# Optimization experiments

Measured on AMD Instinct MI355X. Metric: run time of the kernel, lower is better.

The kernel has to match this reference:

```python
import jax, jax.numpy as jnp
import numpy as np

D_MODEL = 2048
NUM_HEADS = 32
NUM_KV_HEADS = 8
D_K = D_MODEL // NUM_HEADS  # 64
GROUPS = NUM_HEADS // NUM_KV_HEADS  # 4
KV_DIM = NUM_KV_HEADS * D_K  # 512


def setup_inputs() -> dict:
    key = jax.random.key(0)
    ks = jax.random.split(key, 9)
    s = 0.02
    return {
        "x": jax.random.normal(ks[0], (2, 2048, D_MODEL), dtype=jnp.float32),
        "Wq": jax.random.normal(ks[1], (D_MODEL, D_MODEL), dtype=jnp.float32) * s,
        "bq": jnp.zeros((D_MODEL,), dtype=jnp.float32),
        "Wk": jax.random.normal(ks[2], (D_MODEL, KV_DIM), dtype=jnp.float32) * s,
        "bk": jnp.zeros((KV_DIM,), dtype=jnp.float32),
        "Wv": jax.random.normal(ks[3], (D_MODEL, KV_DIM), dtype=jnp.float32) * s,
        "bv": jnp.zeros((KV_DIM,), dtype=jnp.float32),
        "Wo": jax.random.normal(ks[4], (D_MODEL, D_MODEL), dtype=jnp.float32) * s,
        "bo": jnp.zeros((D_MODEL,), dtype=jnp.float32),
    }


def reference(x, Wq, bq, Wk, bk, Wv, bv, Wo, bo):
    B, S, _ = x.shape
    # projections
    Q = (x @ Wq + bq).reshape(B, S, NUM_HEADS, D_K).transpose(0, 2, 1, 3)      # [B,H,S,dk]
    K = (x @ Wk + bk).reshape(B, S, NUM_KV_HEADS, D_K).transpose(0, 2, 1, 3)   # [B,Hkv,S,dk]
    V = (x @ Wv + bv).reshape(B, S, NUM_KV_HEADS, D_K).transpose(0, 2, 1, 3)
    # repeat_interleave KV heads to match query heads
    K = jnp.repeat(K, GROUPS, axis=1)  # [B,H,S,dk]
    V = jnp.repeat(V, GROUPS, axis=1)
    scale = 1.0 / jnp.sqrt(jnp.asarray(D_K, dtype=x.dtype))
    scores = jnp.einsum("bhqd,bhkd->bhqk", Q, K) * scale  # [B,H,S,S]
    attn = jax.nn.softmax(scores, axis=-1)
    out = jnp.einsum("bhqk,bhkd->bhqd", attn, V)           # [B,H,S,dk]
    out = out.transpose(0, 2, 1, 3).reshape(B, S, D_MODEL)
    return out @ Wo + bo
```

## Files before the change

kernel.cpp:

```cpp
#include <hip/hip_runtime.h>
#include <hip/hip_bf16.h>
#include <stdint.h>

typedef __bf16 bf16;
typedef __bf16 bf16x8 __attribute__((ext_vector_type(8)));
typedef float  f32x2  __attribute__((ext_vector_type(2)));
typedef float  f32x4  __attribute__((ext_vector_type(4)));
typedef float  f32x16 __attribute__((ext_vector_type(16)));

#define D_MODEL 2048
#define KV_DIM  512
#define SEQ     2048
#define BATCH   2
#define MTOT    (BATCH*SEQ)
#define QKV_N   3072
#define QSCALE  (0.125f*1.44269504088896f)

#if __has_builtin(__builtin_amdgcn_exp2f)
#define EXP2(x) __builtin_amdgcn_exp2f(x)
#else
#define EXP2(x) exp2f(x)
#endif

__global__ __launch_bounds__(256) void cvt_f32_bf16(const float* __restrict__ in,
                                                    bf16* __restrict__ out, int n) {
  int i = (blockIdx.x * 256 + threadIdx.x) * 4;
  if (i < n) {
    float4 v = *reinterpret_cast<const float4*>(in + i);
    bf16 o[4] = {(bf16)v.x, (bf16)v.y, (bf16)v.z, (bf16)v.w};
    *reinterpret_cast<uint64_t*>(out + i) = *reinterpret_cast<const uint64_t*>(o);
  }
}

__global__ __launch_bounds__(256) void transpose_all(
    const float* __restrict__ Wq, const float* __restrict__ Wk,
    const float* __restrict__ Wv, const float* __restrict__ Wo,
    bf16* __restrict__ Wall, bf16* __restrict__ Wot) {
  const int z = blockIdx.z;
  const float* W; bf16* dst; int N;
  if (z == 0)      { W = Wq; dst = Wall;                          N = 2048; }
  else if (z == 1) { W = Wk; dst = Wall + (size_t)2048 * 2048;    N = 512;  }
  else if (z == 2) { W = Wv; dst = Wall + (size_t)2560 * 2048;    N = 512;  }
  else             { W = Wo; dst = Wot;                           N = 2048; }
  const int n0 = blockIdx.x * 64, k0 = blockIdx.y * 64;
  if (n0 >= N) return;
  __shared__ float tile[64][65];
  const int tx = threadIdx.x & 63;
  const int ty = threadIdx.x >> 6;
  #pragma unroll
  for (int i = ty; i < 64; i += 4)
    tile[i][tx] = W[(size_t)(k0 + i) * N + n0 + tx];
  __syncthreads();
  #pragma unroll
  for (int i = ty; i < 64; i += 4)
    dst[(size_t)(n0 + i) * 2048 + k0 + tx] = (bf16)tile[tx][i];
}

__global__ __launch_bounds__(256) void transpose_v(const bf16* __restrict__ QKV,
                                                   bf16* __restrict__ Vtg) {
  __shared__ bf16 t[64][72];
  const int st = blockIdx.x;
  const int bk = blockIdx.y;
  const int b = bk >> 3, kvh = bk & 7;
  const int tid = threadIdx.x;
  const int r = tid >> 2, c = (tid & 3) * 16;
  const bf16* src = QKV + (size_t)(b * SEQ + st * 64 + r) * QKV_N + 2560 + kvh * 64 + c;
  *(bf16x8*)&t[r][c]     = *(const bf16x8*)src;
  *(bf16x8*)&t[r][c + 8] = *(const bf16x8*)(src + 8);
  __syncthreads();
  bf16 tmp[16];
  #pragma unroll
  for (int j = 0; j < 16; ++j) tmp[j] = t[c + j][r];
  bf16* dst = Vtg + (size_t)(bk * 64 + r) * SEQ + st * 64 + c;
  *(bf16x8*)dst       = *(const bf16x8*)tmp;
  *(bf16x8*)(dst + 8) = *(const bf16x8*)(tmp + 8);
}

__device__ __forceinline__ void gload_lds16(const bf16* g, bf16* l) {
  __builtin_amdgcn_global_load_lds(
      (const __attribute__((address_space(1))) uint32_t*)g,
      (__attribute__((address_space(3))) uint32_t*)l, 16, 0, 0);
}

__device__ __forceinline__ uint32_t pk2(float a, float b) {
  union { bf16 h[2]; uint32_t u; } v;
  v.h[0] = (bf16)a; v.h[1] = (bf16)b;
  return v.u;
}

template<int OUT_BF16>
__global__ __launch_bounds__(256) void gemm_bt(
    const bf16* __restrict__ A, const bf16* __restrict__ Bt,
    const float* __restrict__ b0, const float* __restrict__ b1,
    const float* __restrict__ b2, int sp1, int sp2, int nscale, float scale,
    void* __restrict__ Cout, int M, int N, int K)
{
  __shared__ bf16 As[128 * 64];
  __shared__ bf16 Bs[128 * 64];
  const int tid  = threadIdx.x;
  const int lane = tid & 63;
  const int wid  = tid >> 6;
  const int wr = wid >> 1, wc = wid & 1;
  const int m0 = blockIdx.y * 128, n0 = blockIdx.x * 128;

  f32x4 acc[4][4] = {};

  const int srow = lane >> 3;
  const int scol = (lane & 7) * 8;

  for (int k0 = 0; k0 < K; k0 += 64) {
    #pragma unroll
    for (int i = 0; i < 4; ++i) {
      const int c = wid * 4 + i;
      gload_lds16(A  + (size_t)(m0 + c * 8 + srow) * K + k0 + scol, &As[c * 512]);
      gload_lds16(Bt + (size_t)(n0 + c * 8 + srow) * K + k0 + scol, &Bs[c * 512]);
    }
    __syncthreads();
    #pragma unroll
    for (int kk = 0; kk < 2; ++kk) {
      bf16x8 af[4], bfr[4];
      #pragma unroll
      for (int m = 0; m < 4; ++m)
        af[m] = *reinterpret_cast<const bf16x8*>(
            &As[(wr * 64 + m * 16 + (lane & 15)) * 64 + kk * 32 + (lane >> 4) * 8]);
      #pragma unroll
      for (int n = 0; n < 4; ++n)
        bfr[n] = *reinterpret_cast<const bf16x8*>(
            &Bs[(wc * 64 + n * 16 + (lane & 15)) * 64 + kk * 32 + (lane >> 4) * 8]);
      __builtin_amdgcn_s_setprio(1);
      #pragma unroll
      for (int m = 0; m < 4; ++m)
        #pragma unroll
        for (int n = 0; n < 4; ++n)
          acc[m][n] = __builtin_amdgcn_mfma_f32_16x16x32_bf16(af[m], bfr[n], acc[m][n], 0, 0, 0);
      __builtin_amdgcn_s_setprio(0);
    }
    __syncthreads();
  }

  const int rbase = m0 + wr * 64 + (lane >> 4) * 4;
  const int cbase = n0 + wc * 64 + (lane & 15);
  #pragma unroll
  for (int n = 0; n < 4; ++n) {
    const int col = cbase + n * 16;
    float bv;
    if (col < sp1)      bv = b0[col];
    else if (col < sp2) bv = b1[col - sp1];
    else                bv = b2[col - sp2];
    const float scl = (col < nscale) ? scale : 1.0f;
    #pragma unroll
    for (int m = 0; m < 4; ++m) {
      const int rb = rbase + m * 16;
      #pragma unroll
      for (int r = 0; r < 4; ++r) {
        const float v = (acc[m][n][r] + bv) * scl;
        if (OUT_BF16) ((bf16*)Cout)[(size_t)(rb + r) * N + col] = (bf16)v;
        else          ((float*)Cout)[(size_t)(rb + r) * N + col] = v;
      }
    }
  }
}

__global__ __launch_bounds__(256) void attn_kernel(
    const bf16* __restrict__ QKV, const bf16* __restrict__ Vtg, bf16* __restrict__ ctx)
{
  __shared__ bf16 smem[4][64 * 64];

  const int tid = threadIdx.x, lane = tid & 63, wid = tid >> 6;
  const int l31 = lane & 31, hi = lane >> 5;
  const int qt = blockIdx.x & 15;
  const int bh = blockIdx.x >> 4;
  const int h = bh & 31, b = bh >> 5, kvh = h >> 2;

  const bf16* gK = QKV + (size_t)b * SEQ * QKV_N + 2048 + kvh * 64;
  const bf16* gV = Vtg + (size_t)(b * 8 + kvh) * 64 * SEQ;

  const int sr  = lane >> 3;
  const int scn = (lane & 7) ^ sr;

  bf16x8 qf[4];
  {
    const bf16* qp = QKV + (size_t)(b * SEQ + qt * 128 + wid * 32 + l31) * QKV_N + h * 64 + hi * 8;
    #pragma unroll
    for (int kt = 0; kt < 4; ++kt) qf[kt] = *(const bf16x8*)(qp + kt * 16);
  }

  bf16x8 onesv;
  #pragma unroll
  for (int j = 0; j < 8; ++j) onesv[j] = (bf16)1.0f;

  f32x16 o0 = {}, o1 = {};
  f32x16 lacc = {};

  const int row0 = (wid * 2 + 0) * 8 + sr;
  const int row1 = (wid * 2 + 1) * 8 + sr;
  const bf16* pK0 = gK + (size_t)row0 * QKV_N + scn * 8;
  const bf16* pK1 = gK + (size_t)row1 * QKV_N + scn * 8;
  const bf16* pV0 = gV + (size_t)row0 * SEQ + scn * 8;
  const bf16* pV1 = gV + (size_t)row1 * SEQ + scn * 8;

  gload_lds16(pK0, &smem[0][(wid * 2 + 0) * 512]);
  gload_lds16(pK1, &smem[0][(wid * 2 + 1) * 512]);
  gload_lds16(pV0, &smem[2][(wid * 2 + 0) * 512]);
  gload_lds16(pV1, &smem[2][(wid * 2 + 1) * 512]);
  pK0 += (size_t)64 * QKV_N; pK1 += (size_t)64 * QKV_N; pV0 += 64; pV1 += 64;
  __syncthreads();

  const int rx = l31 & 7;

  for (int it = 0; it < 32; ++it) {
    const int cur = it & 1;
    if (it < 31) {
      gload_lds16(pK0, &smem[cur ^ 1][(wid * 2 + 0) * 512]);
      gload_lds16(pK1, &smem[cur ^ 1][(wid * 2 + 1) * 512]);
      gload_lds16(pV0, &smem[2 + (cur ^ 1)][(wid * 2 + 0) * 512]);
      gload_lds16(pV1, &smem[2 + (cur ^ 1)][(wid * 2 + 1) * 512]);
      pK0 += (size_t)64 * QKV_N; pK1 += (size_t)64 * QKV_N; pV0 += 64; pV1 += 64;
    }
    const bf16* Kb = smem[cur];
    const bf16* Vb = smem[2 + cur];

    bf16x8 kf[8];
    #pragma unroll
    for (int kt = 0; kt < 4; ++kt) {
      const int ck = hi + 2 * kt;
      kf[kt]     = *(const bf16x8*)(Kb + (size_t)l31 * 64        + ((ck ^ rx) * 8));
      kf[kt + 4] = *(const bf16x8*)(Kb + (size_t)(32 + l31) * 64 + ((ck ^ rx) * 8));
    }
    f32x16 s0v = {}, s1v = {};
    __builtin_amdgcn_s_setprio(1);
    #pragma unroll
    for (int kt = 0; kt < 4; ++kt) {
      s0v = __builtin_amdgcn_mfma_f32_32x32x16_bf16(kf[kt],     qf[kt], s0v, 0, 0, 0);
      s1v = __builtin_amdgcn_mfma_f32_32x32x16_bf16(kf[kt + 4], qf[kt], s1v, 0, 0, 0);
    }
    __builtin_amdgcn_s_setprio(0);

    bf16x8 vf[8];
    #pragma unroll
    for (int s = 0; s < 4; ++s) {
      const int ck = hi + 2 * s;
      vf[s]     = *(const bf16x8*)(Vb + (size_t)l31 * 64        + ((ck ^ rx) * 8));
      vf[s + 4] = *(const bf16x8*)(Vb + (size_t)(32 + l31) * 64 + ((ck ^ rx) * 8));
    }

    #pragma unroll
    for (int r = 0; r < 16; ++r) { s0v[r] = EXP2(s0v[r]); s1v[r] = EXP2(s1v[r]); }

    #pragma unroll
    for (int s = 0; s < 4; ++s) {
      const f32x16& sv = (s < 2) ? s0v : s1v;
      const int rb = (s & 1) * 8;
      uint32_t Aw = pk2(sv[rb + 0], sv[rb + 1]);
      uint32_t Bw = pk2(sv[rb + 2], sv[rb + 3]);
      uint32_t Cw = pk2(sv[rb + 4], sv[rb + 5]);
      uint32_t Dw = pk2(sv[rb + 6], sv[rb + 7]);
      union { uint32_t w[4]; bf16x8 v; } pf;
#if __has_builtin(__builtin_amdgcn_permlane32_swap)
      auto rA = __builtin_amdgcn_permlane32_swap(Aw, Cw, false, false);
      auto rB = __builtin_amdgcn_permlane32_swap(Bw, Dw, false, false);
      pf.w[0] = rA[0]; pf.w[1] = rB[0]; pf.w[2] = rA[1]; pf.w[3] = rB[1];
#else
      uint32_t U = hi ? Aw : Cw;
      uint32_t W = hi ? Bw : Dw;
      uint32_t pU = (uint32_t)__shfl_xor((int)U, 32);
      uint32_t pW = (uint32_t)__shfl_xor((int)W, 32);
      pf.w[0] = hi ? pU : Aw;
      pf.w[1] = hi ? pW : Bw;
      pf.w[2] = hi ? Cw : pU;
      pf.w[3] = hi ? Dw : pW;
#endif
      __builtin_amdgcn_s_setprio(1);
      o0 = __builtin_amdgcn_mfma_f32_32x32x16_bf16(vf[s],     pf.v, o0, 0, 0, 0);
      o1 = __builtin_amdgcn_mfma_f32_32x32x16_bf16(vf[s + 4], pf.v, o1, 0, 0, 0);
      lacc = __builtin_amdgcn_mfma_f32_32x32x16_bf16(onesv,   pf.v, lacc, 0, 0, 0);
      __builtin_amdgcn_s_setprio(0);
    }
    __syncthreads();
  }

  const float inv = 1.0f / lacc[0];
  o0 *= inv; o1 *= inv;

  uint32_t* ot = (uint32_t*)((bf16*)smem + wid * 2304);
  #pragma unroll
  for (int r = 0; r < 16; r += 2) {
    const int d = (r & 3) + 8 * (r >> 2) + 4 * hi;
    ot[l31 * 36 + (d >> 1)]        = pk2(o0[r], o0[r + 1]);
    ot[l31 * 36 + ((32 + d) >> 1)] = pk2(o1[r], o1[r + 1]);
  }
  __syncthreads();
  {
    const int q2 = lane >> 1, hf = lane & 1;
    const bf16* src = (const bf16*)smem + wid * 2304 + q2 * 72 + hf * 32;
    bf16* dst = ctx + (size_t)(b * SEQ + qt * 128 + wid * 32 + q2) * D_MODEL + h * 64 + hf * 32;
    #pragma unroll
    for (int k = 0; k < 4; ++k)
      *(bf16x8*)(dst + k * 8) = *(const bf16x8*)(src + k * 8);
  }
}

extern "C" void kernel_launch(void* const* d_in, const int* in_sizes, int n_in,
                              void* d_out, int out_size, void* d_ws, size_t ws_size,
                              hipStream_t stream) {
  const float* x  = (const float*)d_in[0];
  const float* Wq = (const float*)d_in[1];
  const float* bq = (const float*)d_in[2];
  const float* Wk = (const float*)d_in[3];
  const float* bk = (const float*)d_in[4];
  const float* Wv = (const float*)d_in[5];
  const float* bv = (const float*)d_in[6];
  const float* Wo = (const float*)d_in[7];
  const float* bo = (const float*)d_in[8];
  float* out = (float*)d_out;

  char* ws = (char*)d_ws;
  size_t off = 0;
  bf16* xb   = (bf16*)(ws + off); off += (size_t)MTOT * D_MODEL * 2;
  bf16* Wall = (bf16*)(ws + off); off += (size_t)QKV_N * D_MODEL * 2;
  bf16* Wot  = (bf16*)(ws + off); off += (size_t)D_MODEL * D_MODEL * 2;
  bf16* QKV  = (bf16*)(ws + off); off += (size_t)MTOT * QKV_N * 2;
  bf16* ctx  = (bf16*)(ws + off); off += (size_t)MTOT * D_MODEL * 2;
  bf16* Vtg  = (bf16*)(ws + off); off += (size_t)16 * 64 * SEQ * 2;

  {
    int n = MTOT * D_MODEL;
    cvt_f32_bf16<<<n / 4 / 256, 256, 0, stream>>>(x, xb, n);
  }
  transpose_all<<<dim3(32, 32, 4), 256, 0, stream>>>(Wq, Wk, Wv, Wo, Wall, Wot);

  gemm_bt<1><<<dim3(QKV_N / 128, MTOT / 128), 256, 0, stream>>>(
      xb, Wall, bq, bk, bv, 2048, 2560, 2048, QSCALE, QKV, MTOT, QKV_N, D_MODEL);

  transpose_v<<<dim3(SEQ / 64, 16), 256, 0, stream>>>(QKV, Vtg);

  attn_kernel<<<dim3((SEQ / 128) * BATCH * 32), 256, 0, stream>>>(QKV, Vtg, ctx);

  gemm_bt<0><<<dim3(D_MODEL / 128, MTOT / 128), 256, 0, stream>>>(
      ctx, Wot, bo, bo, bo, 2048, 2048, 0, 1.0f, out, MTOT, D_MODEL, D_MODEL);
}
```

Measured before the change: 244.7 us.

## Fuse V transpose into QKV GEMM epilogue and compute softmax denominator on VALU

The QKV GEMM epilogue now writes V-column tiles transposed through shared memory straight into the Vtg layout, which removes the separate transpose_v kernel launch and its extra read/write of V. In the attention loop, the ones-vector MFMA that accumulated the row sum is replaced by a VALU reduction of the exponentiated scores plus a cross-half shuffle. V fragment loads move into the PV loop to lower register pressure, and the first score MFMA now starts from a zero constant. The tradeoff is extra VALU and shuffle work in the attention inner loop and a more complex GEMM epilogue with an extra barrier for V blocks.

```diff
diff --git a/kernel.cpp b/kernel.cpp
--- a/kernel.cpp
+++ b/kernel.cpp
@@ -56,26 +56,6 @@
     dst[(size_t)(n0 + i) * 2048 + k0 + tx] = (bf16)tile[tx][i];
 }
 
-__global__ __launch_bounds__(256) void transpose_v(const bf16* __restrict__ QKV,
-                                                   bf16* __restrict__ Vtg) {
-  __shared__ bf16 t[64][72];
-  const int st = blockIdx.x;
-  const int bk = blockIdx.y;
-  const int b = bk >> 3, kvh = bk & 7;
-  const int tid = threadIdx.x;
-  const int r = tid >> 2, c = (tid & 3) * 16;
-  const bf16* src = QKV + (size_t)(b * SEQ + st * 64 + r) * QKV_N + 2560 + kvh * 64 + c;
-  *(bf16x8*)&t[r][c]     = *(const bf16x8*)src;
-  *(bf16x8*)&t[r][c + 8] = *(const bf16x8*)(src + 8);
-  __syncthreads();
-  bf16 tmp[16];
-  #pragma unroll
-  for (int j = 0; j < 16; ++j) tmp[j] = t[c + j][r];
-  bf16* dst = Vtg + (size_t)(bk * 64 + r) * SEQ + st * 64 + c;
-  *(bf16x8*)dst       = *(const bf16x8*)tmp;
-  *(bf16x8*)(dst + 8) = *(const bf16x8*)(tmp + 8);
-}
-
 __device__ __forceinline__ void gload_lds16(const bf16* g, bf16* l) {
   __builtin_amdgcn_global_load_lds(
       (const __attribute__((address_space(1))) uint32_t*)g,
@@ -93,10 +73,11 @@
     const bf16* __restrict__ A, const bf16* __restrict__ Bt,
     const float* __restrict__ b0, const float* __restrict__ b1,
     const float* __restrict__ b2, int sp1, int sp2, int nscale, float scale,
-    void* __restrict__ Cout, int M, int N, int K)
+    void* __restrict__ Cout, bf16* __restrict__ vt_out, int M, int N, int K)
 {
-  __shared__ bf16 As[128 * 64];
-  __shared__ bf16 Bs[128 * 64];
+  __shared__ bf16 sAB[2][128 * 64];
+  bf16* As = sAB[0];
+  bf16* Bs = sAB[1];
   const int tid  = threadIdx.x;
   const int lane = tid & 63;
   const int wid  = tid >> 6;
@@ -138,26 +119,56 @@
     __syncthreads();
   }
 
+  const bool vblock = (vt_out != nullptr) && (n0 >= sp2);
   const int rbase = m0 + wr * 64 + (lane >> 4) * 4;
   const int cbase = n0 + wc * 64 + (lane & 15);
-  #pragma unroll
-  for (int n = 0; n < 4; ++n) {
-    const int col = cbase + n * 16;
-    float bv;
-    if (col < sp1)      bv = b0[col];
-    else if (col < sp2) bv = b1[col - sp1];
-    else                bv = b2[col - sp2];
-    const float scl = (col < nscale) ? scale : 1.0f;
-    #pragma unroll
-    for (int m = 0; m < 4; ++m) {
-      const int rb = rbase + m * 16;
-      #pragma unroll
-      for (int r = 0; r < 4; ++r) {
-        const float v = (acc[m][n][r] + bv) * scl;
-        if (OUT_BF16) ((bf16*)Cout)[(size_t)(rb + r) * N + col] = (bf16)v;
-        else          ((float*)Cout)[(size_t)(rb + r) * N + col] = v;
+
+  if (!vblock) {
+    #pragma unroll
+    for (int n = 0; n < 4; ++n) {
+      const int col = cbase + n * 16;
+      float bv;
+      if (col < sp1)      bv = b0[col];
+      else if (col < sp2) bv = b1[col - sp1];
+      else                bv = b2[col - sp2];
+      const float scl = (col < nscale) ? scale : 1.0f;
+      #pragma unroll
+      for (int m = 0; m < 4; ++m) {
+        const int rb = rbase + m * 16;
+        #pragma unroll
+        for (int r = 0; r < 4; ++r) {
+          const float v = (acc[m][n][r] + bv) * scl;
+          if (OUT_BF16) ((bf16*)Cout)[(size_t)(rb + r) * N + col] = (bf16)v;
+          else          ((float*)Cout)[(size_t)(rb + r) * N + col] = v;
+        }
       }
     }
+  } else {
+    bf16* tr = &sAB[0][0];
+    #pragma unroll
+    for (int n = 0; n < 4; ++n) {
+      const int col = cbase + n * 16;
+      const float bv = b2[col - sp2];
+      const int cl = wc * 64 + n * 16 + (lane & 15);
+      #pragma unroll
+      for (int m = 0; m < 4; ++m) {
+        const int rl = wr * 64 + m * 16 + (lane >> 4) * 4;
+        #pragma unroll
+        for (int r = 0; r < 4; ++r)
+          tr[cl * 128 + rl + r] = (bf16)(acc[m][n][r] + bv);
+      }
+    }
+    __syncthreads();
+    const int cl = tid & 127, half = tid >> 7;
+    const int g  = n0 - sp2 + cl;
+    const int kvh = g >> 6, dd = g & 63;
+    const int bb = m0 >> 11;
+    const int tok0 = (m0 & 2047) + half * 64;
+    const bf16* src = tr + cl * 128 + half * 64;
+    bf16* dst = vt_out + ((size_t)(bb * 8 + kvh) * 64 + dd) * SEQ + tok0;
+    #pragma unroll
+    for (int k = 0; k < 8; ++k)
+      *(bf16x8*)(dst + k * 8) = *(const bf16x8*)(src + k * 8);
   }
 }
 
@@ -185,12 +196,9 @@
     for (int kt = 0; kt < 4; ++kt) qf[kt] = *(const bf16x8*)(qp + kt * 16);
   }
 
-  bf16x8 onesv;
-  #pragma unroll
-  for (int j = 0; j < 8; ++j) onesv[j] = (bf16)1.0f;
-
+  const f32x16 fz = {};
   f32x16 o0 = {}, o1 = {};
-  f32x16 lacc = {};
+  float lrun = 0.f;
 
   const int row0 = (wid * 2 + 0) * 8 + sr;
   const int row1 = (wid * 2 + 1) * 8 + sr;
@@ -227,25 +235,29 @@
       kf[kt]     = *(const bf16x8*)(Kb + (size_t)l31 * 64        + ((ck ^ rx) * 8));
       kf[kt + 4] = *(const bf16x8*)(Kb + (size_t)(32 + l31) * 64 + ((ck ^ rx) * 8));
     }
-    f32x16 s0v = {}, s1v = {};
     __builtin_amdgcn_s_setprio(1);
-    #pragma unroll
-    for (int kt = 0; kt < 4; ++kt) {
+    f32x16 s0v = __builtin_amdgcn_mfma_f32_32x32x16_bf16(kf[0], qf[0], fz, 0, 0, 0);
+    f32x16 s1v = __builtin_amdgcn_mfma_f32_32x32x16_bf16(kf[4], qf[0], fz, 0, 0, 0);
+    #pragma unroll
+    for (int kt = 1; kt < 4; ++kt) {
       s0v = __builtin_amdgcn_mfma_f32_32x32x16_bf16(kf[kt],     qf[kt], s0v, 0, 0, 0);
       s1v = __builtin_amdgcn_mfma_f32_32x32x16_bf16(kf[kt + 4], qf[kt], s1v, 0, 0, 0);
     }
     __builtin_amdgcn_s_setprio(0);
 
-    bf16x8 vf[8];
-    #pragma unroll
-    for (int s = 0; s < 4; ++s) {
-      const int ck = hi + 2 * s;
-      vf[s]     = *(const bf16x8*)(Vb + (size_t)l31 * 64        + ((ck ^ rx) * 8));
-      vf[s + 4] = *(const bf16x8*)(Vb + (size_t)(32 + l31) * 64 + ((ck ^ rx) * 8));
-    }
-
     #pragma unroll
     for (int r = 0; r < 16; ++r) { s0v[r] = EXP2(s0v[r]); s1v[r] = EXP2(s1v[r]); }
+
+    {
+      f32x16 ps = s0v + s1v;
+      #pragma unroll
+      for (int r = 0; r < 8; ++r) ps[r] += ps[r + 8];
+      #pragma unroll
+      for (int r = 0; r < 4; ++r) ps[r] += ps[r + 4];
+      float rs = (ps[0] + ps[2]) + (ps[1] + ps[3]);
+      rs += __shfl_xor(rs, 32);
+      lrun += rs;
+    }
 
     #pragma unroll
     for (int s = 0; s < 4; ++s) {
@@ -270,16 +282,18 @@
       pf.w[2] = hi ? Cw : pU;
       pf.w[3] = hi ? Dw : pW;
 #endif
+      const int ck = hi + 2 * s;
+      bf16x8 v0 = *(const bf16x8*)(Vb + (size_t)l31 * 64        + ((ck ^ rx) * 8));
+      bf16x8 v1 = *(const bf16x8*)(Vb + (size_t)(32 + l31) * 64 + ((ck ^ rx) * 8));
       __builtin_amdgcn_s_setprio(1);
-      o0 = __builtin_amdgcn_mfma_f32_32x32x16_bf16(vf[s],     pf.v, o0, 0, 0, 0);
-      o1 = __builtin_amdgcn_mfma_f32_32x32x16_bf16(vf[s + 4], pf.v, o1, 0, 0, 0);
-      lacc = __builtin_amdgcn_mfma_f32_32x32x16_bf16(onesv,   pf.v, lacc, 0, 0, 0);
+      o0 = __builtin_amdgcn_mfma_f32_32x32x16_bf16(v0, pf.v, o0, 0, 0, 0);
+      o1 = __builtin_amdgcn_mfma_f32_32x32x16_bf16(v1, pf.v, o1, 0, 0, 0);
       __builtin_amdgcn_s_setprio(0);
     }
     __syncthreads();
   }
 
-  const float inv = 1.0f / lacc[0];
+  const float inv = 1.0f / lrun;
   o0 *= inv; o1 *= inv;
 
   uint32_t* ot = (uint32_t*)((bf16*)smem + wid * 2304);
@@ -330,12 +344,10 @@
   transpose_all<<<dim3(32, 32, 4), 256, 0, stream>>>(Wq, Wk, Wv, Wo, Wall, Wot);
 
   gemm_bt<1><<<dim3(QKV_N / 128, MTOT / 128), 256, 0, stream>>>(
-      xb, Wall, bq, bk, bv, 2048, 2560, 2048, QSCALE, QKV, MTOT, QKV_N, D_MODEL);
-
-  transpose_v<<<dim3(SEQ / 64, 16), 256, 0, stream>>>(QKV, Vtg);
+      xb, Wall, bq, bk, bv, 2048, 2560, 2048, QSCALE, QKV, Vtg, MTOT, QKV_N, D_MODEL);
 
   attn_kernel<<<dim3((SEQ / 128) * BATCH * 32), 256, 0, stream>>>(QKV, Vtg, ctx);
 
   gemm_bt<0><<<dim3(D_MODEL / 128, MTOT / 128), 256, 0, stream>>>(
-      ctx, Wot, bo, bo, bo, 2048, 2048, 0, 1.0f, out, MTOT, D_MODEL, D_MODEL);
-}
+      ctx, Wot, bo, bo, bo, 2048, 2048, 0, 1.0f, out, nullptr, MTOT, D_MODEL, D_MODEL);
+}
```

Measured after the change: 271.2 us. 10.8% more time.

## Replace GEMMs with 256-row double-buffered swizzled LDS kernel using 512 threads

Applied to the files above, without the earlier changes.

Replaces the 128x128 single-buffered GEMM with a 256-row tile kernel (192 or 128 columns) run by 8 waves. It double-buffers LDS with explicit vmcnt waits so global loads overlap MFMA work, and XOR-swizzles LDS chunks to avoid bank conflicts. Block IDs are remapped for L2 locality, and the tiles are sized so each GEMM launches exactly 256 blocks. The aim is better data reuse and latency hiding; the hand-set waitcnt values are fragile, and the larger LDS footprint lowers occupancy.

```diff
diff --git a/kernel.cpp b/kernel.cpp
--- a/kernel.cpp
+++ b/kernel.cpp
@@ -88,68 +88,119 @@
   return v.u;
 }
 
-template<int OUT_BF16>
-__global__ __launch_bounds__(256) void gemm_bt(
+template<int NF, int OUT_BF16>
+__global__ void gemm256(
     const bf16* __restrict__ A, const bf16* __restrict__ Bt,
     const float* __restrict__ b0, const float* __restrict__ b1,
     const float* __restrict__ b2, int sp1, int sp2, int nscale, float scale,
-    void* __restrict__ Cout, int M, int N, int K)
+    void* __restrict__ Cout, int N, int K)
 {
-  __shared__ bf16 As[128 * 64];
-  __shared__ bf16 Bs[128 * 64];
-  const int tid  = threadIdx.x;
-  const int lane = tid & 63;
-  const int wid  = tid >> 6;
-  const int wr = wid >> 1, wc = wid & 1;
-  const int m0 = blockIdx.y * 128, n0 = blockIdx.x * 128;
-
-  f32x4 acc[4][4] = {};
-
-  const int srow = lane >> 3;
-  const int scol = (lane & 7) * 8;
-
-  for (int k0 = 0; k0 < K; k0 += 64) {
-    #pragma unroll
-    for (int i = 0; i < 4; ++i) {
-      const int c = wid * 4 + i;
-      gload_lds16(A  + (size_t)(m0 + c * 8 + srow) * K + k0 + scol, &As[c * 512]);
-      gload_lds16(Bt + (size_t)(n0 + c * 8 + srow) * K + k0 + scol, &Bs[c * 512]);
-    }
-    __syncthreads();
-    #pragma unroll
-    for (int kk = 0; kk < 2; ++kk) {
-      bf16x8 af[4], bfr[4];
-      #pragma unroll
-      for (int m = 0; m < 4; ++m)
-        af[m] = *reinterpret_cast<const bf16x8*>(
-            &As[(wr * 64 + m * 16 + (lane & 15)) * 64 + kk * 32 + (lane >> 4) * 8]);
-      #pragma unroll
-      for (int n = 0; n < 4; ++n)
-        bfr[n] = *reinterpret_cast<const bf16x8*>(
-            &Bs[(wc * 64 + n * 16 + (lane & 15)) * 64 + kk * 32 + (lane >> 4) * 8]);
-      __builtin_amdgcn_s_setprio(1);
-      #pragma unroll
-      for (int m = 0; m < 4; ++m)
-        #pragma unroll
-        for (int n = 0; n < 4; ++n)
-          acc[m][n] = __builtin_amdgcn_mfma_f32_16x16x32_bf16(af[m], bfr[n], acc[m][n], 0, 0, 0);
-      __builtin_amdgcn_s_setprio(0);
-    }
-    __syncthreads();
-  }
-
-  const int rbase = m0 + wr * 64 + (lane >> 4) * 4;
-  const int cbase = n0 + wc * 64 + (lane & 15);
-  #pragma unroll
-  for (int n = 0; n < 4; ++n) {
-    const int col = cbase + n * 16;
+  __shared__ bf16 As[2][256 * 64];
+  __shared__ bf16 Bs[2][NF * 64 * 64];
+
+  const int tid = threadIdx.x, lane = tid & 63;
+  const int wid = tid >> 6;
+  const int wr = wid >> 2, wc = wid & 3;
+  const int l15 = lane & 15, hi = lane >> 4;
+  const int rx = l15 & 7;
+
+  const int bid = blockIdx.y * 16 + blockIdx.x;
+  const int swz = (bid & 7) * 32 + (bid >> 3);
+  const int m0 = (swz >> 4) * 256, n0 = (swz & 15) * (NF * 16 * 4);
+
+  const int srow = tid >> 3;
+  const int schk = (tid & 7) ^ (srow & 7);
+  const bf16* aSrc = A  + (size_t)(m0 + srow) * K + schk * 8;
+  const bf16* bSrc = Bt + (size_t)(n0 + srow) * K + schk * 8;
+  const size_t rstep = (size_t)64 * K;
+
+  f32x4 acc[8][NF] = {};
+
+  const int NT = K / 64;
+
+#define G256_STAGE(T, BUF)                                            \
+  {                                                                   \
+    const bf16* a_ = aSrc + (T) * 64;                                 \
+    _Pragma("unroll")                                                 \
+    for (int j = 0; j < 4; ++j)                                       \
+      gload_lds16(a_ + j * rstep, &As[BUF][j * 4096 + tid * 8]);      \
+    const bf16* b_ = bSrc + (T) * 64;                                 \
+    _Pragma("unroll")                                                 \
+    for (int j = 0; j < NF; ++j)                                      \
+      gload_lds16(b_ + j * rstep, &Bs[BUF][j * 4096 + tid * 8]);      \
+  }
+
+#define G256_WAITL()                                                  \
+  if constexpr (NF == 3) asm volatile("s_waitcnt vmcnt(7)" ::: "memory"); \
+  else                   asm volatile("s_waitcnt vmcnt(6)" ::: "memory");
+
+#define G256_BODY(BUF)                                                \
+  {                                                                   \
+    _Pragma("unroll")                                                 \
+    for (int kk = 0; kk < 2; ++kk) {                                  \
+      bf16x8 af[8], bfv[NF];                                          \
+      _Pragma("unroll")                                               \
+      for (int m = 0; m < 8; ++m)                                     \
+        af[m] = *(const bf16x8*)&As[BUF][(wr * 128 + m * 16 + l15) * 64 \
+                                         + ((kk * 4 + hi) ^ rx) * 8];  \
+      _Pragma("unroll")                                               \
+      for (int n = 0; n < NF; ++n)                                    \
+        bfv[n] = *(const bf16x8*)&Bs[BUF][(wc * (NF * 16) + n * 16 + l15) * 64 \
+                                          + ((kk * 4 + hi) ^ rx) * 8]; \
+      __builtin_amdgcn_s_setprio(1);                                  \
+      _Pragma("unroll")                                               \
+      for (int m = 0; m < 8; ++m)                                     \
+        _Pragma("unroll")                                             \
+        for (int n = 0; n < NF; ++n)                                  \
+          acc[m][n] = __builtin_amdgcn_mfma_f32_16x16x32_bf16(        \
+              af[m], bfv[n], acc[m][n], 0, 0, 0);                     \
+      __builtin_amdgcn_s_setprio(0);                                  \
+    }                                                                 \
+  }
+
+  G256_STAGE(0, 0)
+  G256_STAGE(1, 1)
+  G256_WAITL()
+  __builtin_amdgcn_sched_barrier(0);
+  __builtin_amdgcn_s_barrier();
+  __builtin_amdgcn_sched_barrier(0);
+
+  for (int t = 0; t < NT; t += 2) {
+    #pragma unroll
+    for (int u = 0; u < 2; ++u) {
+      G256_BODY(u)
+      __builtin_amdgcn_sched_barrier(0);
+      __builtin_amdgcn_s_barrier();
+      __builtin_amdgcn_sched_barrier(0);
+      const int tt = t + u;
+      if (tt < NT - 2) {
+        G256_STAGE(tt + 2, u)
+        G256_WAITL()
+      } else {
+        asm volatile("s_waitcnt vmcnt(0)" ::: "memory");
+      }
+      __builtin_amdgcn_sched_barrier(0);
+      __builtin_amdgcn_s_barrier();
+      __builtin_amdgcn_sched_barrier(0);
+    }
+  }
+
+#undef G256_STAGE
+#undef G256_WAITL
+#undef G256_BODY
+
+  const int rbase = m0 + wr * 128 + hi * 4;
+  const int cb = n0 + wc * (NF * 16) + l15;
+  #pragma unroll
+  for (int n = 0; n < NF; ++n) {
+    const int col = cb + n * 16;
     float bv;
     if (col < sp1)      bv = b0[col];
     else if (col < sp2) bv = b1[col - sp1];
     else                bv = b2[col - sp2];
     const float scl = (col < nscale) ? scale : 1.0f;
     #pragma unroll
-    for (int m = 0; m < 4; ++m) {
+    for (int m = 0; m < 8; ++m) {
       const int rb = rbase + m * 16;
       #pragma unroll
       for (int r = 0; r < 4; ++r) {
@@ -329,13 +380,13 @@
   }
   transpose_all<<<dim3(32, 32, 4), 256, 0, stream>>>(Wq, Wk, Wv, Wo, Wall, Wot);
 
-  gemm_bt<1><<<dim3(QKV_N / 128, MTOT / 128), 256, 0, stream>>>(
-      xb, Wall, bq, bk, bv, 2048, 2560, 2048, QSCALE, QKV, MTOT, QKV_N, D_MODEL);
+  gemm256<3, 1><<<dim3(16, 16), 512, 0, stream>>>(
+      xb, Wall, bq, bk, bv, 2048, 2560, 2048, QSCALE, QKV, QKV_N, D_MODEL);
 
   transpose_v<<<dim3(SEQ / 64, 16), 256, 0, stream>>>(QKV, Vtg);
 
   attn_kernel<<<dim3((SEQ / 128) * BATCH * 32), 256, 0, stream>>>(QKV, Vtg, ctx);
 
-  gemm_bt<0><<<dim3(D_MODEL / 128, MTOT / 128), 256, 0, stream>>>(
-      ctx, Wot, bo, bo, bo, 2048, 2048, 0, 1.0f, out, MTOT, D_MODEL, D_MODEL);
-}
+  gemm256<2, 0><<<dim3(16, 16), 512, 0, stream>>>(
+      ctx, Wot, bo, bo, bo, 2048, 2048, 0, 1.0f, out, D_MODEL, D_MODEL);
+}
```

Result: slower. 707.3 us (+189.0%).
